# Optimization experiments

Measured on AMD Instinct MI355X. Metric: run time of the kernel, lower is better.

## Reference

```python
import jax, jax.numpy as jnp
import numpy as np

B, N, H, O = 2, 512, 128, 32  # batch, n_particles, hidden_dim, obs_dim


def _linear_init(key, out_d, in_d):
    kw, kb = jax.random.split(key)
    s = 1.0 / np.sqrt(in_d)
    W = jax.random.uniform(kw, (out_d, in_d), minval=-s, maxval=s, dtype=jnp.float32)
    b = jax.random.uniform(kb, (out_d,), minval=-s, maxval=s, dtype=jnp.float32)
    return W, b


def setup_inputs() -> dict:
    key = jax.random.key(0)
    ks = jax.random.split(key, 8)
    z = jax.random.normal(ks[0], (B, N, H), dtype=jnp.float32)
    s_t = jax.random.normal(ks[1], (B, N, O), dtype=jnp.float32)
    W1, b1 = _linear_init(ks[2], H, 2 * H)   # relation_mlp layer 0
    W2, b2 = _linear_init(ks[3], H, H)       # relation_mlp layer 2
    Wq, bq = _linear_init(ks[4], H, H)       # query_proj
    Wk, bk = _linear_init(ks[5], H, O)       # key_proj
    W3, b3 = _linear_init(ks[6], H, H)       # aggregation_mlp layer 0
    W4, b4 = _linear_init(ks[7], H, H)       # aggregation_mlp layer 2
    return dict(z=z, s_t=s_t, W1=W1, b1=b1, W2=W2, b2=b2, Wq=Wq, bq=bq,
                Wk=Wk, bk=bk, W3=W3, b3=b3, W4=W4, b4=b4)


def reference(z, s_t, W1, b1, W2, b2, Wq, bq, Wk, bk, W3, b3, W4, b4):
    b_, n, h = z.shape
    # query depends only on i, key only on j (repeat in the original is redundant)
    q = z @ Wq.T + bq            # [B,N,H]
    k = s_t @ Wk.T + bk          # [B,N,H]
    scores = jnp.einsum('bih,bjh->bij', q, k) / (h ** 0.5)   # [B,N,N]
    eye = jnp.eye(n, dtype=bool)
    scores = jnp.where(eye, -jnp.inf, scores)
    attn = jax.nn.softmax(scores, axis=-1)                   # [B,N,N]
    # relation_mlp on concat(z_i, z_j): split first weight into i- and j- halves
    W1i, W1j = W1[:, :h], W1[:, h:]
    zi = z @ W1i.T               # [B,N,H]
    zj = z @ W1j.T               # [B,N,H]
    rel = jnp.tanh(zi[:, :, None, :] + zj[:, None, :, :] + b1) @ W2.T + b2  # [B,N,N,H]
    agg = jnp.einsum('bij,bijh->bih', attn, rel)             # weighted sum over j
    dz_dt = jnp.tanh(agg @ W3.T + b3) @ W4.T + b4
    return dz_dt
```

## Files before the change

kernel.cpp:

```cpp
#include <hip/hip_runtime.h>
#include <hip/hip_bf16.h>

#define NN 512
#define HH 128
#define OO 32

#define KL 2.8853900817779268f

__device__ __forceinline__ float vexp2(float x) {
    float r; asm("v_exp_f32 %0, %1" : "=v"(r) : "v"(x)); return r;
}
__device__ __forceinline__ float vrcp(float x) {
    float r; asm("v_rcp_f32 %0, %1" : "=v"(r) : "v"(x)); return r;
}
__device__ __forceinline__ float tanh_fast(float x) {
    float e = vexp2(KL * x);
    return 1.0f - 2.0f * vrcp(e + 1.0f);
}
__device__ __forceinline__ float waveRedMax(float v) {
#pragma unroll
    for (int off = 32; off > 0; off >>= 1) v = fmaxf(v, __shfl_xor(v, off, 64));
    return v;
}
__device__ __forceinline__ float waveRedSum(float v) {
#pragma unroll
    for (int off = 32; off > 0; off >>= 1) v += __shfl_xor(v, off, 64);
    return v;
}
__device__ __forceinline__ float red8(float v) {
    v += __shfl_xor(v, 1, 64); v += __shfl_xor(v, 2, 64); v += __shfl_xor(v, 4, 64);
    return v;
}
__device__ __forceinline__ float dot16(const float4* w, const float* x) {
    float a = 0;
#pragma unroll
    for (int i = 0; i < 4; i++) {
        float4 xv = *(const float4*)(x + i * 4);
        a = fmaf(xv.x, w[i].x, a); a = fmaf(xv.y, w[i].y, a);
        a = fmaf(xv.z, w[i].z, a); a = fmaf(xv.w, w[i].w, a);
    }
    return a;
}

__global__ __launch_bounds__(1024, 8) void prep_kernel(
    const float* __restrict__ z, const float* __restrict__ s_t,
    const float* __restrict__ W1, const float* __restrict__ b1,
    const float* __restrict__ Wq, const float* __restrict__ bq,
    const float* __restrict__ Wk, const float* __restrict__ bk,
    float* __restrict__ qG, float* __restrict__ EziG,
    float* __restrict__ EzjG, float* __restrict__ kTG) {
    __shared__ float zrow[2][HH];
    __shared__ float srow[2][OO];
    int t = threadIdx.x;
    int r0 = blockIdx.x * 2;
    if (t < 2 * HH) zrow[t >> 7][t & 127] = z[(size_t)r0 * HH + t];
    else if (t < 2 * HH + 2 * OO) {
        int u = t - 2 * HH;
        srow[u >> 5][u & 31] = s_t[(size_t)r0 * OO + u];
    }
    __syncthreads();

    int kq = t & 7, h = t >> 3;
    float vbq = bq[h], vb1 = b1[h], vbk = bk[h];
    float4 w[4];

    {
        const float4* Wp = (const float4*)(Wq + (size_t)h * HH) + kq * 4;
#pragma unroll
        for (int i = 0; i < 4; i++) w[i] = Wp[i];
        float a0 = dot16(w, &zrow[0][kq * 16]);
        float a1 = dot16(w, &zrow[1][kq * 16]);
        a0 = red8(a0); a1 = red8(a1);
        if (kq == 0) {
            qG[(size_t)r0 * HH + h] = a0 + vbq;
            qG[(size_t)(r0 + 1) * HH + h] = a1 + vbq;
        }
    }
    {
        const float4* Wp = (const float4*)(W1 + (size_t)h * 2 * HH) + kq * 4;
#pragma unroll
        for (int i = 0; i < 4; i++) w[i] = Wp[i];
        float a0 = dot16(w, &zrow[0][kq * 16]);
        float a1 = dot16(w, &zrow[1][kq * 16]);
        a0 = red8(a0); a1 = red8(a1);
        if (kq == 0) {
            EziG[(size_t)r0 * HH + h] = vexp2(KL * (a0 + vb1));
            EziG[(size_t)(r0 + 1) * HH + h] = vexp2(KL * (a1 + vb1));
        }
    }
    {
        const float4* Wp = (const float4*)(W1 + (size_t)h * 2 * HH + HH) + kq * 4;
#pragma unroll
        for (int i = 0; i < 4; i++) w[i] = Wp[i];
        float a0 = dot16(w, &zrow[0][kq * 16]);
        float a1 = dot16(w, &zrow[1][kq * 16]);
        a0 = red8(a0); a1 = red8(a1);
        if (kq == 0) {
            EzjG[(size_t)r0 * HH + h] = vexp2(KL * a0);
            EzjG[(size_t)(r0 + 1) * HH + h] = vexp2(KL * a1);
        }
    }
    {
        float4 wk = ((const float4*)(Wk + (size_t)h * OO))[kq];
        float4 s0 = *(const float4*)&srow[0][kq * 4];
        float4 s1 = *(const float4*)&srow[1][kq * 4];
        float a0 = s0.x * wk.x + s0.y * wk.y + s0.z * wk.z + s0.w * wk.w;
        float a1 = s1.x * wk.x + s1.y * wk.y + s1.z * wk.z + s1.w * wk.w;
        a0 = red8(a0); a1 = red8(a1);
        if (kq == 0) {
            int b0 = r0 >> 9, j0 = r0 & 511;
            kTG[((size_t)b0 * HH + h) * NN + j0] = a0 + vbk;
            int b1_ = (r0 + 1) >> 9, j1 = (r0 + 1) & 511;
            kTG[((size_t)b1_ * HH + h) * NN + j1] = a1 + vbk;
        }
    }
}

__global__ __launch_bounds__(1024, 8) void fused_kernel(
    const float* __restrict__ qG, const float* __restrict__ kTG,
    const float* __restrict__ EziG, const float* __restrict__ EzjG,
    const float* __restrict__ W2, const float* __restrict__ b2,
    const float* __restrict__ W3, const float* __restrict__ b3,
    const float* __restrict__ W4, const float* __restrict__ b4,
    float* __restrict__ out) {
    __shared__ float q2T[HH][2];
    __shared__ float c2T[HH][2];
    __shared__ float attnT[NN][2];
    __shared__ float scp[2][2][NN];
    __shared__ float part[16][2][HH];
    __shared__ float UL[2][HH];
    __shared__ float aggL[2][HH];
    __shared__ float h1L[2][HH];
    __shared__ float redA[16], redB[16];

    int t = threadIdx.x;
    int bid = blockIdx.x;
    int b = bid >> 8;
    int i0 = (bid & 255) * 2;
    int r0 = bid * 2;

    if (t < 256)      { int h = t >> 1, r = t & 1; q2T[h][r] = qG[(size_t)(r0 + r) * HH + h]; }
    else if (t < 512) { int u = t - 256, h = u >> 1, r = u & 1; c2T[h][r] = EziG[(size_t)(r0 + r) * HH + h]; }
    __syncthreads();

    {
        int j = t & 511, hs = t >> 9, h0 = hs * 64;
        const float* kb = kTG + ((size_t)b * HH + h0) * NN + j;
        float s0 = 0, s1 = 0;
#pragma unroll 8
        for (int hh = 0; hh < 64; hh++) {
            float kv = kb[(size_t)hh * NN];
            float2 qv = *(const float2*)q2T[h0 + hh];
            s0 = fmaf(qv.x, kv, s0); s1 = fmaf(qv.y, kv, s1);
        }
        scp[hs][0][j] = s0; scp[hs][1][j] = s1;
    }
    __syncthreads();

    {
        int r = t >> 9, j = t & 511;
        const float sc = 0.08838834764831845f;
        float s = (scp[0][r][j] + scp[1][r][j]) * sc;
        if (j == i0 + r) s = -1e30f;
        int lane = t & 63, w = t >> 6, wb = r * 8;
        float m = waveRedMax(s);
        if (lane == 0) redA[w] = m;
        __syncthreads();
        float mm = redA[wb];
#pragma unroll
        for (int k = 1; k < 8; k++) mm = fmaxf(mm, redA[wb + k]);
        float e = __expf(s - mm);
        float p = waveRedSum(e);
        if (lane == 0) redB[w] = p;
        __syncthreads();
        float S = redB[wb];
#pragma unroll
        for (int k = 1; k < 8; k++) S += redB[wb + k];
        attnT[j][r] = e * __fdividef(1.0f, S);
    }
    __syncthreads();

    {
        int lane6 = t & 63, qs = t >> 6;
        int hp = lane6 * 2;
        float2 cA = *(const float2*)c2T[hp];
        float2 cB = *(const float2*)c2T[hp + 1];
        const float2* zb2 = (const float2*)(EzjG + (size_t)b * NN * HH) + lane6;
        float a0A = 0, a1A = 0, a0B = 0, a1B = 0;
        int jb = qs * 32;
#pragma unroll 8
        for (int jj = 0; jj < 32; jj++) {
            int j = jb + jj;
            float2 E = zb2[(size_t)j * 64];
            float2 w = *(const float2*)attnT[j];
            a0A = fmaf(w.x, vrcp(fmaf(cA.x, E.x, 1.0f)), a0A);
            a1A = fmaf(w.y, vrcp(fmaf(cA.y, E.x, 1.0f)), a1A);
            a0B = fmaf(w.x, vrcp(fmaf(cB.x, E.y, 1.0f)), a0B);
            a1B = fmaf(w.y, vrcp(fmaf(cB.y, E.y, 1.0f)), a1B);
        }
        *(float2*)&part[qs][0][hp] = make_float2(a0A, a0B);
        *(float2*)&part[qs][1][hp] = make_float2(a1A, a1B);
    }
    __syncthreads();
    if (t < 256) {
        int r = t >> 7, h = t & 127;
        float s = 0;
#pragma unroll
        for (int q = 0; q < 16; q++) s += part[q][r][h];
        UL[r][h] = fmaf(-2.0f, s, 1.0f);
    }
    __syncthreads();

    {
        int kq = t & 7, h = t >> 3;
        float vb2 = b2[h], vb3 = b3[h], vb4 = b4[h];
        float4 w[4];
        {
            const float4* Wp = (const float4*)(W2 + (size_t)h * HH) + kq * 4;
#pragma unroll
            for (int i = 0; i < 4; i++) w[i] = Wp[i];
            float a0 = dot16(w, &UL[0][kq * 16]);
            float a1 = dot16(w, &UL[1][kq * 16]);
            a0 = red8(a0); a1 = red8(a1);
            if (kq == 0) { aggL[0][h] = a0 + vb2; aggL[1][h] = a1 + vb2; }
        }
        __syncthreads();
        {
            const float4* Wp = (const float4*)(W3 + (size_t)h * HH) + kq * 4;
#pragma unroll
            for (int i = 0; i < 4; i++) w[i] = Wp[i];
            float a0 = dot16(w, &aggL[0][kq * 16]);
            float a1 = dot16(w, &aggL[1][kq * 16]);
            a0 = red8(a0); a1 = red8(a1);
            if (kq == 0) { h1L[0][h] = tanh_fast(a0 + vb3); h1L[1][h] = tanh_fast(a1 + vb3); }
        }
        __syncthreads();
        {
            const float4* Wp = (const float4*)(W4 + (size_t)h * HH) + kq * 4;
#pragma unroll
            for (int i = 0; i < 4; i++) w[i] = Wp[i];
            float a0 = dot16(w, &h1L[0][kq * 16]);
            float a1 = dot16(w, &h1L[1][kq * 16]);
            a0 = red8(a0); a1 = red8(a1);
            if (kq == 0) {
                out[(size_t)r0 * HH + h] = a0 + vb4;
                out[(size_t)(r0 + 1) * HH + h] = a1 + vb4;
            }
        }
    }
}

extern "C" void kernel_launch(void* const* d_in, const int* in_sizes, int n_in,
                              void* d_out, int out_size, void* d_ws, size_t ws_size,
                              hipStream_t stream) {
    const float* z   = (const float*)d_in[0];
    const float* s_t = (const float*)d_in[1];
    const float* W1  = (const float*)d_in[2];
    const float* b1  = (const float*)d_in[3];
    const float* W2  = (const float*)d_in[4];
    const float* b2  = (const float*)d_in[5];
    const float* Wq  = (const float*)d_in[6];
    const float* bq  = (const float*)d_in[7];
    const float* Wk  = (const float*)d_in[8];
    const float* bk  = (const float*)d_in[9];
    const float* W3  = (const float*)d_in[10];
    const float* b3  = (const float*)d_in[11];
    const float* W4  = (const float*)d_in[12];
    const float* b4  = (const float*)d_in[13];
    float* out = (float*)d_out;

    float* ws  = (float*)d_ws;
    float* qG  = ws;
    float* kT  = ws + 131072;
    float* Ezi = ws + 262144;
    float* Ezj = ws + 393216;

    hipLaunchKernelGGL(prep_kernel, dim3(512), dim3(1024), 0, stream,
                       z, s_t, W1, b1, Wq, bq, Wk, bk, qG, Ezi, Ezj, kT);
    hipLaunchKernelGGL(fused_kernel, dim3(512), dim3(1024), 0, stream,
                       qG, kT, Ezi, Ezj, W2, b2, W3, b3, W4, b4, out);
}
```

Before: 40.82 us.

## Process four query rows per block and pack q/c buffers per block

Each block now handles four rows instead of two, halving the grid to 256 blocks. Each loaded key column, Ezj row and weight row is reused across twice as many rows. Shared memory for the score partials and the aggregation partials is aliased into one buffer, with an extra barrier added. The prep kernel writes q and exp(c) in a block-packed transposed layout so the main kernel can load them contiguously. The cost is fewer blocks, which may underfill the 256 CUs, and more registers per thread.

After: 32.98 us. 19.2% less time.

```diff
diff --git a/kernel.cpp b/kernel.cpp
--- a/kernel.cpp
+++ b/kernel.cpp
@@ -42,20 +42,21 @@
     return a;
 }
 
-__global__ __launch_bounds__(1024, 8) void prep_kernel(
+__global__ __launch_bounds__(1024, 4) void prep_kernel(
     const float* __restrict__ z, const float* __restrict__ s_t,
     const float* __restrict__ W1, const float* __restrict__ b1,
     const float* __restrict__ Wq, const float* __restrict__ bq,
     const float* __restrict__ Wk, const float* __restrict__ bk,
-    float* __restrict__ qG, float* __restrict__ EziG,
+    float* __restrict__ qP, float* __restrict__ cP,
     float* __restrict__ EzjG, float* __restrict__ kTG) {
-    __shared__ float zrow[2][HH];
-    __shared__ float srow[2][OO];
+    __shared__ float zrow[4][HH];
+    __shared__ float srow[4][OO];
     int t = threadIdx.x;
-    int r0 = blockIdx.x * 2;
-    if (t < 2 * HH) zrow[t >> 7][t & 127] = z[(size_t)r0 * HH + t];
-    else if (t < 2 * HH + 2 * OO) {
-        int u = t - 2 * HH;
+    int bid = blockIdx.x;
+    int r0 = bid * 4;
+    if (t < 4 * HH) zrow[t >> 7][t & 127] = z[(size_t)r0 * HH + t];
+    else if (t < 4 * HH + 4 * OO) {
+        int u = t - 4 * HH;
         srow[u >> 5][u & 31] = s_t[(size_t)r0 * OO + u];
     }
     __syncthreads();
@@ -63,146 +64,172 @@
     int kq = t & 7, h = t >> 3;
     float vbq = bq[h], vb1 = b1[h], vbk = bk[h];
     float4 w[4];
+    float a0, a1, a2, a3;
 
     {
         const float4* Wp = (const float4*)(Wq + (size_t)h * HH) + kq * 4;
 #pragma unroll
         for (int i = 0; i < 4; i++) w[i] = Wp[i];
-        float a0 = dot16(w, &zrow[0][kq * 16]);
-        float a1 = dot16(w, &zrow[1][kq * 16]);
-        a0 = red8(a0); a1 = red8(a1);
+        a0 = red8(dot16(w, &zrow[0][kq * 16]));
+        a1 = red8(dot16(w, &zrow[1][kq * 16]));
+        a2 = red8(dot16(w, &zrow[2][kq * 16]));
+        a3 = red8(dot16(w, &zrow[3][kq * 16]));
         if (kq == 0) {
-            qG[(size_t)r0 * HH + h] = a0 + vbq;
-            qG[(size_t)(r0 + 1) * HH + h] = a1 + vbq;
+            float* qp = qP + (size_t)bid * 512 + h * 4;
+            qp[0] = a0 + vbq; qp[1] = a1 + vbq; qp[2] = a2 + vbq; qp[3] = a3 + vbq;
         }
     }
     {
         const float4* Wp = (const float4*)(W1 + (size_t)h * 2 * HH) + kq * 4;
 #pragma unroll
         for (int i = 0; i < 4; i++) w[i] = Wp[i];
-        float a0 = dot16(w, &zrow[0][kq * 16]);
-        float a1 = dot16(w, &zrow[1][kq * 16]);
-        a0 = red8(a0); a1 = red8(a1);
+        a0 = red8(dot16(w, &zrow[0][kq * 16]));
+        a1 = red8(dot16(w, &zrow[1][kq * 16]));
+        a2 = red8(dot16(w, &zrow[2][kq * 16]));
+        a3 = red8(dot16(w, &zrow[3][kq * 16]));
         if (kq == 0) {
-            EziG[(size_t)r0 * HH + h] = vexp2(KL * (a0 + vb1));
-            EziG[(size_t)(r0 + 1) * HH + h] = vexp2(KL * (a1 + vb1));
+            float* cp = cP + (size_t)bid * 512 + h * 4;
+            cp[0] = vexp2(KL * (a0 + vb1)); cp[1] = vexp2(KL * (a1 + vb1));
+            cp[2] = vexp2(KL * (a2 + vb1)); cp[3] = vexp2(KL * (a3 + vb1));
         }
     }
     {
         const float4* Wp = (const float4*)(W1 + (size_t)h * 2 * HH + HH) + kq * 4;
 #pragma unroll
         for (int i = 0; i < 4; i++) w[i] = Wp[i];
-        float a0 = dot16(w, &zrow[0][kq * 16]);
-        float a1 = dot16(w, &zrow[1][kq * 16]);
-        a0 = red8(a0); a1 = red8(a1);
+        a0 = red8(dot16(w, &zrow[0][kq * 16]));
+        a1 = red8(dot16(w, &zrow[1][kq * 16]));
+        a2 = red8(dot16(w, &zrow[2][kq * 16]));
+        a3 = red8(dot16(w, &zrow[3][kq * 16]));
         if (kq == 0) {
-            EzjG[(size_t)r0 * HH + h] = vexp2(KL * a0);
+            EzjG[(size_t)(r0 + 0) * HH + h] = vexp2(KL * a0);
             EzjG[(size_t)(r0 + 1) * HH + h] = vexp2(KL * a1);
+            EzjG[(size_t)(r0 + 2) * HH + h] = vexp2(KL * a2);
+            EzjG[(size_t)(r0 + 3) * HH + h] = vexp2(KL * a3);
         }
     }
     {
         float4 wk = ((const float4*)(Wk + (size_t)h * OO))[kq];
         float4 s0 = *(const float4*)&srow[0][kq * 4];
         float4 s1 = *(const float4*)&srow[1][kq * 4];
-        float a0 = s0.x * wk.x + s0.y * wk.y + s0.z * wk.z + s0.w * wk.w;
-        float a1 = s1.x * wk.x + s1.y * wk.y + s1.z * wk.z + s1.w * wk.w;
-        a0 = red8(a0); a1 = red8(a1);
+        float4 s2 = *(const float4*)&srow[2][kq * 4];
+        float4 s3 = *(const float4*)&srow[3][kq * 4];
+        a0 = red8(s0.x * wk.x + s0.y * wk.y + s0.z * wk.z + s0.w * wk.w);
+        a1 = red8(s1.x * wk.x + s1.y * wk.y + s1.z * wk.z + s1.w * wk.w);
+        a2 = red8(s2.x * wk.x + s2.y * wk.y + s2.z * wk.z + s2.w * wk.w);
+        a3 = red8(s3.x * wk.x + s3.y * wk.y + s3.z * wk.z + s3.w * wk.w);
         if (kq == 0) {
-            int b0 = r0 >> 9, j0 = r0 & 511;
-            kTG[((size_t)b0 * HH + h) * NN + j0] = a0 + vbk;
-            int b1_ = (r0 + 1) >> 9, j1 = (r0 + 1) & 511;
-            kTG[((size_t)b1_ * HH + h) * NN + j1] = a1 + vbk;
-        }
-    }
-}
-
-__global__ __launch_bounds__(1024, 8) void fused_kernel(
-    const float* __restrict__ qG, const float* __restrict__ kTG,
-    const float* __restrict__ EziG, const float* __restrict__ EzjG,
+            int b = r0 >> 9, j0 = r0 & 511;
+            float* kp = kTG + ((size_t)b * HH + h) * NN + j0;
+            kp[0] = a0 + vbk; kp[1] = a1 + vbk; kp[2] = a2 + vbk; kp[3] = a3 + vbk;
+        }
+    }
+}
+
+__global__ __launch_bounds__(1024, 4) void fused_kernel(
+    const float* __restrict__ qP, const float* __restrict__ kTG,
+    const float* __restrict__ cP, const float* __restrict__ EzjG,
     const float* __restrict__ W2, const float* __restrict__ b2,
     const float* __restrict__ W3, const float* __restrict__ b3,
     const float* __restrict__ W4, const float* __restrict__ b4,
     float* __restrict__ out) {
-    __shared__ float q2T[HH][2];
-    __shared__ float c2T[HH][2];
-    __shared__ float attnT[NN][2];
-    __shared__ float scp[2][2][NN];
-    __shared__ float part[16][2][HH];
-    __shared__ float UL[2][HH];
-    __shared__ float aggL[2][HH];
-    __shared__ float h1L[2][HH];
+    __shared__ float q4T[HH][4];
+    __shared__ float c4T[HH][4];
+    __shared__ float attnT[NN][4];
+    __shared__ float buf[8192];
+    __shared__ float UL[4][HH];
+    __shared__ float aggL[4][HH];
+    __shared__ float h1L[4][HH];
     __shared__ float redA[16], redB[16];
+
+    float (*scp)[4][NN] = (float (*)[4][NN])buf;
+    float (*part)[4][HH] = (float (*)[4][HH])buf;
 
     int t = threadIdx.x;
     int bid = blockIdx.x;
-    int b = bid >> 8;
-    int i0 = (bid & 255) * 2;
-    int r0 = bid * 2;
-
-    if (t < 256)      { int h = t >> 1, r = t & 1; q2T[h][r] = qG[(size_t)(r0 + r) * HH + h]; }
-    else if (t < 512) { int u = t - 256, h = u >> 1, r = u & 1; c2T[h][r] = EziG[(size_t)(r0 + r) * HH + h]; }
+    int b = bid >> 7;
+    int i0 = (bid & 127) * 4;
+    int r0 = bid * 4;
+
+    if (t < 512)       ((float*)q4T)[t] = qP[(size_t)bid * 512 + t];
+    else               ((float*)c4T)[t - 512] = cP[(size_t)bid * 512 + (t - 512)];
     __syncthreads();
 
     {
         int j = t & 511, hs = t >> 9, h0 = hs * 64;
         const float* kb = kTG + ((size_t)b * HH + h0) * NN + j;
-        float s0 = 0, s1 = 0;
+        float s0 = 0, s1 = 0, s2 = 0, s3 = 0;
 #pragma unroll 8
         for (int hh = 0; hh < 64; hh++) {
             float kv = kb[(size_t)hh * NN];
-            float2 qv = *(const float2*)q2T[h0 + hh];
+            float4 qv = *(const float4*)q4T[h0 + hh];
             s0 = fmaf(qv.x, kv, s0); s1 = fmaf(qv.y, kv, s1);
+            s2 = fmaf(qv.z, kv, s2); s3 = fmaf(qv.w, kv, s3);
         }
         scp[hs][0][j] = s0; scp[hs][1][j] = s1;
-    }
-    __syncthreads();
-
-    {
-        int r = t >> 9, j = t & 511;
+        scp[hs][2][j] = s2; scp[hs][3][j] = s3;
+    }
+    __syncthreads();
+
+    {
+        int rp = t >> 9, j = t & 511;
+        int lr0 = rp * 2, lr1 = lr0 + 1;
         const float sc = 0.08838834764831845f;
-        float s = (scp[0][r][j] + scp[1][r][j]) * sc;
-        if (j == i0 + r) s = -1e30f;
-        int lane = t & 63, w = t >> 6, wb = r * 8;
-        float m = waveRedMax(s);
-        if (lane == 0) redA[w] = m;
-        __syncthreads();
-        float mm = redA[wb];
-#pragma unroll
-        for (int k = 1; k < 8; k++) mm = fmaxf(mm, redA[wb + k]);
-        float e = __expf(s - mm);
-        float p = waveRedSum(e);
-        if (lane == 0) redB[w] = p;
-        __syncthreads();
-        float S = redB[wb];
-#pragma unroll
-        for (int k = 1; k < 8; k++) S += redB[wb + k];
-        attnT[j][r] = e * __fdividef(1.0f, S);
+        float s0 = (scp[0][lr0][j] + scp[1][lr0][j]) * sc;
+        float s1 = (scp[0][lr1][j] + scp[1][lr1][j]) * sc;
+        if (j == i0 + lr0) s0 = -1e30f;
+        if (j == i0 + lr1) s1 = -1e30f;
+        int lane = t & 63, w = t >> 6, wb = rp * 8;
+        float m0 = waveRedMax(s0), m1 = waveRedMax(s1);
+        if (lane == 0) { redA[w] = m0; redB[w] = m1; }
+        __syncthreads();
+        float mm0 = redA[wb], mm1 = redB[wb];
+#pragma unroll
+        for (int k = 1; k < 8; k++) { mm0 = fmaxf(mm0, redA[wb + k]); mm1 = fmaxf(mm1, redB[wb + k]); }
+        float e0 = __expf(s0 - mm0), e1 = __expf(s1 - mm1);
+        float p0 = waveRedSum(e0), p1 = waveRedSum(e1);
+        __syncthreads();
+        if (lane == 0) { redA[w] = p0; redB[w] = p1; }
+        __syncthreads();
+        float S0 = redA[wb], S1 = redB[wb];
+#pragma unroll
+        for (int k = 1; k < 8; k++) { S0 += redA[wb + k]; S1 += redB[wb + k]; }
+        attnT[j][lr0] = e0 * __fdividef(1.0f, S0);
+        attnT[j][lr1] = e1 * __fdividef(1.0f, S1);
     }
     __syncthreads();
 
     {
         int lane6 = t & 63, qs = t >> 6;
         int hp = lane6 * 2;
-        float2 cA = *(const float2*)c2T[hp];
-        float2 cB = *(const float2*)c2T[hp + 1];
+        float4 cA = *(const float4*)c4T[hp];
+        float4 cB = *(const float4*)c4T[hp + 1];
         const float2* zb2 = (const float2*)(EzjG + (size_t)b * NN * HH) + lane6;
-        float a0A = 0, a1A = 0, a0B = 0, a1B = 0;
+        float a0A = 0, a1A = 0, a2A = 0, a3A = 0;
+        float a0B = 0, a1B = 0, a2B = 0, a3B = 0;
         int jb = qs * 32;
 #pragma unroll 8
         for (int jj = 0; jj < 32; jj++) {
             int j = jb + jj;
             float2 E = zb2[(size_t)j * 64];
-            float2 w = *(const float2*)attnT[j];
+            float4 w = *(const float4*)attnT[j];
             a0A = fmaf(w.x, vrcp(fmaf(cA.x, E.x, 1.0f)), a0A);
             a1A = fmaf(w.y, vrcp(fmaf(cA.y, E.x, 1.0f)), a1A);
+            a2A = fmaf(w.z, vrcp(fmaf(cA.z, E.x, 1.0f)), a2A);
+            a3A = fmaf(w.w, vrcp(fmaf(cA.w, E.x, 1.0f)), a3A);
             a0B = fmaf(w.x, vrcp(fmaf(cB.x, E.y, 1.0f)), a0B);
             a1B = fmaf(w.y, vrcp(fmaf(cB.y, E.y, 1.0f)), a1B);
-        }
+            a2B = fmaf(w.z, vrcp(fmaf(cB.z, E.y, 1.0f)), a2B);
+            a3B = fmaf(w.w, vrcp(fmaf(cB.w, E.y, 1.0f)), a3B);
+        }
+        __syncthreads();
         *(float2*)&part[qs][0][hp] = make_float2(a0A, a0B);
         *(float2*)&part[qs][1][hp] = make_float2(a1A, a1B);
-    }
-    __syncthreads();
-    if (t < 256) {
+        *(float2*)&part[qs][2][hp] = make_float2(a2A, a2B);
+        *(float2*)&part[qs][3][hp] = make_float2(a3A, a3B);
+    }
+    __syncthreads();
+    if (t < 512) {
         int r = t >> 7, h = t & 127;
         float s = 0;
 #pragma unroll
@@ -219,32 +246,43 @@
             const float4* Wp = (const float4*)(W2 + (size_t)h * HH) + kq * 4;
 #pragma unroll
             for (int i = 0; i < 4; i++) w[i] = Wp[i];
-            float a0 = dot16(w, &UL[0][kq * 16]);
-            float a1 = dot16(w, &UL[1][kq * 16]);
-            a0 = red8(a0); a1 = red8(a1);
-            if (kq == 0) { aggL[0][h] = a0 + vb2; aggL[1][h] = a1 + vb2; }
+            float a0 = red8(dot16(w, &UL[0][kq * 16]));
+            float a1 = red8(dot16(w, &UL[1][kq * 16]));
+            float a2 = red8(dot16(w, &UL[2][kq * 16]));
+            float a3 = red8(dot16(w, &UL[3][kq * 16]));
+            if (kq == 0) {
+                aggL[0][h] = a0 + vb2; aggL[1][h] = a1 + vb2;
+                aggL[2][h] = a2 + vb2; aggL[3][h] = a3 + vb2;
+            }
         }
         __syncthreads();
         {
             const float4* Wp = (const float4*)(W3 + (size_t)h * HH) + kq * 4;
 #pragma unroll
             for (int i = 0; i < 4; i++) w[i] = Wp[i];
-            float a0 = dot16(w, &aggL[0][kq * 16]);
-            float a1 = dot16(w, &aggL[1][kq * 16]);
-            a0 = red8(a0); a1 = red8(a1);
-            if (kq == 0) { h1L[0][h] = tanh_fast(a0 + vb3); h1L[1][h] = tanh_fast(a1 + vb3); }
+            float a0 = red8(dot16(w, &aggL[0][kq * 16]));
+            float a1 = red8(dot16(w, &aggL[1][kq * 16]));
+            float a2 = red8(dot16(w, &aggL[2][kq * 16]));
+            float a3 = red8(dot16(w, &aggL[3][kq * 16]));
+            if (kq == 0) {
+                h1L[0][h] = tanh_fast(a0 + vb3); h1L[1][h] = tanh_fast(a1 + vb3);
+                h1L[2][h] = tanh_fast(a2 + vb3); h1L[3][h] = tanh_fast(a3 + vb3);
+            }
         }
         __syncthreads();
         {
             const float4* Wp = (const float4*)(W4 + (size_t)h * HH) + kq * 4;
 #pragma unroll
             for (int i = 0; i < 4; i++) w[i] = Wp[i];
-            float a0 = dot16(w, &h1L[0][kq * 16]);
-            float a1 = dot16(w, &h1L[1][kq * 16]);
-            a0 = red8(a0); a1 = red8(a1);
+            float a0 = red8(dot16(w, &h1L[0][kq * 16]));
+            float a1 = red8(dot16(w, &h1L[1][kq * 16]));
+            float a2 = red8(dot16(w, &h1L[2][kq * 16]));
+            float a3 = red8(dot16(w, &h1L[3][kq * 16]));
             if (kq == 0) {
-                out[(size_t)r0 * HH + h] = a0 + vb4;
+                out[(size_t)(r0 + 0) * HH + h] = a0 + vb4;
                 out[(size_t)(r0 + 1) * HH + h] = a1 + vb4;
+                out[(size_t)(r0 + 2) * HH + h] = a2 + vb4;
+                out[(size_t)(r0 + 3) * HH + h] = a3 + vb4;
             }
         }
     }
@@ -270,13 +308,13 @@
     float* out = (float*)d_out;
 
     float* ws  = (float*)d_ws;
-    float* qG  = ws;
+    float* qP  = ws;
     float* kT  = ws + 131072;
-    float* Ezi = ws + 262144;
+    float* cP  = ws + 262144;
     float* Ezj = ws + 393216;
 
-    hipLaunchKernelGGL(prep_kernel, dim3(512), dim3(1024), 0, stream,
-                       z, s_t, W1, b1, Wq, bq, Wk, bk, qG, Ezi, Ezj, kT);
-    hipLaunchKernelGGL(fused_kernel, dim3(512), dim3(1024), 0, stream,
-                       qG, kT, Ezi, Ezj, W2, b2, W3, b3, W4, b4, out);
-}
+    hipLaunchKernelGGL(prep_kernel, dim3(256), dim3(1024), 0, stream,
+                       z, s_t, W1, b1, Wq, bq, Wk, bk, qP, cP, Ezj, kT);
+    hipLaunchKernelGGL(fused_kernel, dim3(256), dim3(1024), 0, stream,
+                       qP, kT, cP, Ezj, W2, b2, W3, b3, W4, b4, out);
+}
```
